# Performance work log

Hardware: AMD Instinct MI355X
Metric: run time of the kernel (lower is better)

## Reference

```python
import jax, jax.numpy as jnp
import numpy as np

NEG_SLOPE = 0.2  # PyG GATConv default negative_slope


def _add_self_loops(edge_index, num_nodes):
    # PyG GATConv add_self_loops=True default
    loop = jnp.arange(num_nodes, dtype=edge_index.dtype)
    src = jnp.concatenate([edge_index[0], loop])
    dst = jnp.concatenate([edge_index[1], loop])
    return src, dst


def _gat_layer(x, src, dst, W, att_src, att_dst, bias, heads, out_ch):
    """One PyG-style GATConv layer (concat=True).
    x: [N, F_in]; W: [F_in, heads*out_ch]; att_*: [heads, out_ch]; bias: [heads*out_ch].
    """
    N = x.shape[0]
    h = (x @ W).reshape(N, heads, out_ch)               # [N, H, C]
    a_src = jnp.einsum('nhc,hc->nh', h, att_src)        # [N, H]
    a_dst = jnp.einsum('nhc,hc->nh', h, att_dst)        # [N, H]
    logits = jax.nn.leaky_relu(a_src[src] + a_dst[dst], NEG_SLOPE)  # [E, H]
    # segment softmax over destination neighborhoods
    m = jax.ops.segment_max(logits, dst, num_segments=N)            # [N, H]
    e = jnp.exp(logits - m[dst])                                     # [E, H]
    s = jax.ops.segment_sum(e, dst, num_segments=N)                  # [N, H]
    alpha = e / s[dst]                                               # [E, H]
    # scatter-aggregate weighted source features
    out = jax.ops.segment_sum(alpha[:, :, None] * h[src], dst, num_segments=N)  # [N, H, C]
    return out.reshape(N, heads * out_ch) + bias


def setup_inputs() -> dict:
    key = jax.random.key(0)
    ks = jax.random.split(key, 10)
    N, E = 50000, 800000
    F_in, HID, H, NC = 128, 64, 4, 10
    x = jax.random.normal(ks[0], (N, F_in), dtype=jnp.float32)
    edge_index = jax.random.randint(ks[1], (2, E), 0, N, dtype=jnp.int64)
    sc1 = 1.0 / np.sqrt(F_in)
    sc2 = 1.0 / np.sqrt(HID * H)
    return {
        'x': x,
        'edge_index': edge_index,
        'W1': jax.random.normal(ks[2], (F_in, H * HID), dtype=jnp.float32) * sc1,
        'att_src1': jax.random.normal(ks[3], (H, HID), dtype=jnp.float32) * sc1,
        'att_dst1': jax.random.normal(ks[4], (H, HID), dtype=jnp.float32) * sc1,
        'b1': jnp.zeros((H * HID,), dtype=jnp.float32),
        'W2': jax.random.normal(ks[5], (H * HID, NC), dtype=jnp.float32) * sc2,
        'att_src2': jax.random.normal(ks[6], (1, NC), dtype=jnp.float32) * sc2,
        'att_dst2': jax.random.normal(ks[7], (1, NC), dtype=jnp.float32) * sc2,
        'b2': jnp.zeros((NC,), dtype=jnp.float32),
    }


def reference(x, edge_index, W1, att_src1, att_dst1, b1, W2, att_src2, att_dst2, b2):
    N = x.shape[0]
    src, dst = _add_self_loops(edge_index, N)
    h = _gat_layer(x, src, dst, W1, att_src1, att_dst1, b1, heads=4, out_ch=64)
    h = jax.nn.elu(h)
    out = _gat_layer(h, src, dst, W2, att_src2, att_dst2, b2, heads=1, out_ch=10)
    return out
```

## Files before the change

### kernel.cpp

```cpp
#include <hip/hip_runtime.h>
#include <hip/hip_fp16.h>
#include <math.h>

#define NEG_SLOPE 0.2f
#define LOG2E 1.44269504088896f

#if __has_builtin(__builtin_amdgcn_exp2f)
#define EXP2(x) __builtin_amdgcn_exp2f(x)
#else
#define EXP2(x) exp2f(x)
#endif

typedef _Float16 half8 __attribute__((ext_vector_type(8)));
typedef float floatx4 __attribute__((ext_vector_type(4)));

__global__ __launch_bounds__(256) void prep1(const float* __restrict__ W1,
                                             half8* __restrict__ Bpack,
                                             int* __restrict__ deg, int N) {
  if (blockIdx.x < 16) {
    int tid = blockIdx.x * 256 + threadIdx.x;
    int l = tid & 63;
    int ksnt = tid >> 6;
    int ks = ksnt & 3;
    int nt = ksnt >> 2;
    int col = nt * 16 + (l & 15);
    int krow = ks * 32 + (l >> 4) * 8;
    half8 v;
#pragma unroll
    for (int j = 0; j < 8; j++) v[j] = (_Float16)W1[(krow + j) * 256 + col];
    Bpack[tid] = v;
  } else {
    int i = (blockIdx.x - 16) * 256 + threadIdx.x;
    if (i < N) deg[i] = 0;
  }
}

__global__ __launch_bounds__(256) void phase2(
    const float* __restrict__ x, const half8* __restrict__ Bpack,
    const float* __restrict__ att_s, const float* __restrict__ att_d,
    __half* __restrict__ h1, float* __restrict__ a1s, float* __restrict__ a1d,
    const int* __restrict__ dst, int* __restrict__ deg, int* __restrict__ rank,
    int N, int E, int gemmBlocks, int histBlocks) {
  if ((int)blockIdx.x >= gemmBlocks) {
    int b = blockIdx.x - gemmBlocks;
    for (int e = b * 256 + threadIdx.x; e < E; e += histBlocks * 256)
      rank[e] = atomicAdd(deg + dst[e], 1);
    return;
  }
  const int wave = threadIdx.x >> 6, lane = threadIdx.x & 63;
  const int quad = lane >> 4, li = lane & 15;
  const int n0 = (blockIdx.x * 4 + wave) * 16;
  if (n0 >= N) return;
  floatx4 acc[16];
#pragma unroll
  for (int t = 0; t < 16; t++) acc[t] = (floatx4){0.f, 0.f, 0.f, 0.f};
  const float* xrow = x + (size_t)(n0 + li) * 128;
#pragma unroll
  for (int ks = 0; ks < 4; ks++) {
    float4 xa = *(const float4*)(xrow + ks * 32 + quad * 8);
    float4 xb = *(const float4*)(xrow + ks * 32 + quad * 8 + 4);
    half8 a;
    a[0] = (_Float16)xa.x; a[1] = (_Float16)xa.y;
    a[2] = (_Float16)xa.z; a[3] = (_Float16)xa.w;
    a[4] = (_Float16)xb.x; a[5] = (_Float16)xb.y;
    a[6] = (_Float16)xb.z; a[7] = (_Float16)xb.w;
#pragma unroll
    for (int nt = 0; nt < 16; nt++) {
      half8 b = Bpack[(nt * 4 + ks) * 64 + lane];
      acc[nt] = __builtin_amdgcn_mfma_f32_16x16x32_f16(a, b, acc[nt], 0, 0, 0);
    }
  }
#pragma unroll
  for (int nt = 0; nt < 16; nt++) {
#pragma unroll
    for (int r = 0; r < 4; r++) {
      h1[(size_t)(n0 + quad * 4 + r) * 256 + nt * 16 + li] = __float2half(acc[nt][r]);
    }
  }
  float as_f[16], ad_f[16];
#pragma unroll
  for (int nt = 0; nt < 16; nt++) {
    as_f[nt] = att_s[nt * 16 + li];
    ad_f[nt] = att_d[nt * 16 + li];
  }
#pragma unroll
  for (int r = 0; r < 4; r++) {
    int node = n0 + quad * 4 + r;
#pragma unroll
    for (int h = 0; h < 4; h++) {
      float vs = 0.f, vd = 0.f;
#pragma unroll
      for (int ntl = 0; ntl < 4; ntl++) {
        int nt = h * 4 + ntl;
        vs = fmaf(acc[nt][r], as_f[nt], vs);
        vd = fmaf(acc[nt][r], ad_f[nt], vd);
      }
#pragma unroll
      for (int off = 8; off > 0; off >>= 1) {
        vs += __shfl_down(vs, off, 16);
        vd += __shfl_down(vd, off, 16);
      }
      if (li == 0) {
        a1s[node * 4 + h] = vs * LOG2E;
        a1d[node * 4 + h] = vd * LOG2E;
      }
    }
  }
}

__global__ void scan_local(const int* __restrict__ deg, int* __restrict__ excl,
                           int* __restrict__ bsum, int N) {
  __shared__ int s[256];
  int i = blockIdx.x * 256 + threadIdx.x;
  int v = (i < N) ? ((deg[i] + 1 + 3) & ~3) : 0;
  s[threadIdx.x] = v;
  __syncthreads();
  for (int off = 1; off < 256; off <<= 1) {
    int t = (threadIdx.x >= off) ? s[threadIdx.x - off] : 0;
    __syncthreads();
    s[threadIdx.x] += t;
    __syncthreads();
  }
  if (i < N) excl[i] = s[threadIdx.x] - v;
  if (threadIdx.x == 255) bsum[blockIdx.x] = s[255];
}

__global__ void scan_add2(const int* __restrict__ excl, const int* __restrict__ bsum,
                          int* __restrict__ rowptr, int* __restrict__ elist,
                          int N, int nb) {
  __shared__ int s[256];
  int v = (threadIdx.x < nb) ? bsum[threadIdx.x] : 0;
  s[threadIdx.x] = v;
  __syncthreads();
  for (int off = 1; off < 256; off <<= 1) {
    int t = (threadIdx.x >= off) ? s[threadIdx.x - off] : 0;
    __syncthreads();
    s[threadIdx.x] += t;
    __syncthreads();
  }
  __syncthreads();
  int base = (blockIdx.x > 0) ? s[blockIdx.x - 1] : 0;
  int i = blockIdx.x * 256 + threadIdx.x;
  if (i < N) {
    int r = excl[i] + base;
    rowptr[i] = r;
    elist[r] = i;
  }
}

__global__ void scatter2(const int* __restrict__ src, const int* __restrict__ dst,
                         const int* __restrict__ rank, const int* __restrict__ rowptr,
                         int* __restrict__ elist, int E) {
  int e = blockIdx.x * 256 + threadIdx.x;
  if (e >= E) return;
  elist[rowptr[dst[e]] + 1 + rank[e]] = src[e];
}

__global__ __launch_bounds__(256) void agg1_fused(
    const int* __restrict__ rowptr, const int* __restrict__ degp,
    const int* __restrict__ elist, const __half* __restrict__ h1,
    const float* __restrict__ a1s, const float* __restrict__ a1d,
    const float* __restrict__ b1, const float* __restrict__ W2,
    const float* __restrict__ as2, const float* __restrict__ ad2,
    __half* __restrict__ h2, float* __restrict__ a2s, float* __restrict__ a2d,
    int N) {
  __shared__ float w2s[64 * 41];
  const int t = threadIdx.x;
  for (int i = t; i < 2560; i += 256) {
    int ch = i / 10, jj = i - ch * 10;
    w2s[(ch >> 2) * 41 + (ch & 3) * 10 + jj] = W2[i];
  }
  __syncthreads();

  const int wave = t >> 6, lane = t & 63;
  const int n = blockIdx.x * 4 + wave;
  if (n >= N) return;
  const int row = rowptr[n];
  const int deg = degp[n] + 1;
  const int* el = elist + row;
  const int hidx = lane >> 4;
  const float adh = a1d[n * 4 + hidx];

  float den = 0.f;
  float acc0 = 0.f, acc1 = 0.f, acc2 = 0.f, acc3 = 0.f;
  int j = 0;
  for (; j + 8 <= deg; j += 8) {
    int4 eA = *(const int4*)(el + j);
    int4 eB = *(const int4*)(el + j + 4);
    int ss[8] = {eA.x, eA.y, eA.z, eA.w, eB.x, eB.y, eB.z, eB.w};
    float lv[8];
    uint2 uv[8];
#pragma unroll
    for (int u = 0; u < 8; u++) {
      lv[u] = a1s[ss[u] * 4 + hidx];
      uv[u] = *(const uint2*)(h1 + (size_t)ss[u] * 256 + lane * 4);
    }
#pragma unroll
    for (int u = 0; u < 8; u++) {
      float l = lv[u] + adh;
      float e = EXP2(fmaxf(l, NEG_SLOPE * l));
      den += e;
      float2 a = __half22float2(*(const __half2*)&uv[u].x);
      float2 b = __half22float2(*(const __half2*)&uv[u].y);
      acc0 = fmaf(e, a.x, acc0); acc1 = fmaf(e, a.y, acc1);
      acc2 = fmaf(e, b.x, acc2); acc3 = fmaf(e, b.y, acc3);
    }
  }
  for (; j + 4 <= deg; j += 4) {
    int4 eA = *(const int4*)(el + j);
    int ss[4] = {eA.x, eA.y, eA.z, eA.w};
    float lv[4];
    uint2 uv[4];
#pragma unroll
    for (int u = 0; u < 4; u++) {
      lv[u] = a1s[ss[u] * 4 + hidx];
      uv[u] = *(const uint2*)(h1 + (size_t)ss[u] * 256 + lane * 4);
    }
#pragma unroll
    for (int u = 0; u < 4; u++) {
      float l = lv[u] + adh;
      float e = EXP2(fmaxf(l, NEG_SLOPE * l));
      den += e;
      float2 a = __half22float2(*(const __half2*)&uv[u].x);
      float2 b = __half22float2(*(const __half2*)&uv[u].y);
      acc0 = fmaf(e, a.x, acc0); acc1 = fmaf(e, a.y, acc1);
      acc2 = fmaf(e, b.x, acc2); acc3 = fmaf(e, b.y, acc3);
    }
  }
  for (; j < deg; j++) {
    int s0 = el[j];
    float l0 = a1s[s0 * 4 + hidx] + adh;
    uint2 u0 = *(const uint2*)(h1 + (size_t)s0 * 256 + lane * 4);
    float e0 = EXP2(fmaxf(l0, NEG_SLOPE * l0));
    den += e0;
    float2 a = __half22float2(*(const __half2*)&u0.x);
    float2 b = __half22float2(*(const __half2*)&u0.y);
    acc0 = fmaf(e0, a.x, acc0); acc1 = fmaf(e0, a.y, acc1);
    acc2 = fmaf(e0, b.x, acc2); acc3 = fmaf(e0, b.y, acc3);
  }

  float inv = 1.0f / den;
  float4 bb = *(const float4*)(b1 + lane * 4);
  float c0 = fmaf(acc0, inv, bb.x);
  float c1 = fmaf(acc1, inv, bb.y);
  float c2 = fmaf(acc2, inv, bb.z);
  float c3 = fmaf(acc3, inv, bb.w);
  c0 = c0 > 0.f ? c0 : expm1f(c0);
  c1 = c1 > 0.f ? c1 : expm1f(c1);
  c2 = c2 > 0.f ? c2 : expm1f(c2);
  c3 = c3 > 0.f ? c3 : expm1f(c3);
  const float* w0 = w2s + lane * 41;
  float p[10];
#pragma unroll
  for (int jj = 0; jj < 10; jj++)
    p[jj] = fmaf(c0, w0[jj], fmaf(c1, w0[10 + jj], fmaf(c2, w0[20 + jj], c3 * w0[30 + jj])));
#pragma unroll
  for (int jj = 0; jj < 10; jj++) {
#pragma unroll
    for (int off = 32; off > 0; off >>= 1) p[jj] += __shfl_down(p[jj], off, 64);
  }
  if (lane == 0) {
    float ds = 0.f, dd = 0.f;
#pragma unroll
    for (int jj = 0; jj < 10; jj++) {
      h2[(size_t)n * 16 + jj] = __float2half(p[jj]);
      ds = fmaf(p[jj], as2[jj], ds);
      dd = fmaf(p[jj], ad2[jj], dd);
    }
    a2s[n] = ds * LOG2E;
    a2d[n] = dd * LOG2E;
  }
}

__global__ __launch_bounds__(256) void agg2_csr(
    const int* __restrict__ rowptr, const int* __restrict__ degp,
    const int* __restrict__ elist, const __half* __restrict__ h2,
    const float* __restrict__ a2s, const float* __restrict__ a2d,
    const float* __restrict__ b2, float* __restrict__ out, int N) {
  int wave = threadIdx.x >> 6, lane = threadIdx.x & 63;
  int n = blockIdx.x * 4 + wave;
  if (n >= N) return;
  int row = rowptr[n];
  int deg = degp[n] + 1;
  const int* el = elist + row;
  float ad = a2d[n];
  int g = lane / 10;
  int c = lane - g * 10;
  float den = 0.f, acc = 0.f;
  if (g < 6) {
    int jj = g;
    for (; jj + 6 < deg; jj += 12) {
      int sA = el[jj], sB = el[jj + 6];
      float lA = a2s[sA] + ad;
      float lB = a2s[sB] + ad;
      __half hA = h2[(size_t)sA * 16 + c];
      __half hB = h2[(size_t)sB * 16 + c];
      float eA = EXP2(fmaxf(lA, NEG_SLOPE * lA));
      float eB = EXP2(fmaxf(lB, NEG_SLOPE * lB));
      den += eA + eB;
      acc = fmaf(eA, __half2float(hA), fmaf(eB, __half2float(hB), acc));
    }
    for (; jj < deg; jj += 6) {
      int s = el[jj];
      float l = a2s[s] + ad;
      float ev = EXP2(fmaxf(l, NEG_SLOPE * l));
      den += ev;
      acc = fmaf(ev, __half2float(h2[(size_t)s * 16 + c]), acc);
    }
  }
  acc += __shfl_down(acc, 30, 64);
  den += __shfl_down(den, 30, 64);
  acc += __shfl_down(acc, 10, 64) + __shfl_down(acc, 20, 64);
  den += __shfl_down(den, 10, 64) + __shfl_down(den, 20, 64);
  if (lane < 10) out[(size_t)n * 10 + lane] = acc / den + b2[lane];
}

extern "C" void kernel_launch(void* const* d_in, const int* in_sizes, int n_in,
                              void* d_out, int out_size, void* d_ws, size_t ws_size,
                              hipStream_t stream) {
  const float* x = (const float*)d_in[0];
  const int* ei = (const int*)d_in[1];
  const float* W1 = (const float*)d_in[2];
  const float* as1 = (const float*)d_in[3];
  const float* ad1 = (const float*)d_in[4];
  const float* b1 = (const float*)d_in[5];
  const float* W2 = (const float*)d_in[6];
  const float* as2 = (const float*)d_in[7];
  const float* ad2 = (const float*)d_in[8];
  const float* b2 = (const float*)d_in[9];
  float* out = (float*)d_out;

  const int N = in_sizes[0] / 128;
  const int E = in_sizes[1] / 2;
  const int* srcp = ei;
  const int* dstp = ei + E;

  char* ws = (char*)d_ws;
  size_t off = 0;
  auto alloc = [&](size_t nbytes) {
    char* p = ws + off;
    off += (nbytes + 255) & ~(size_t)255;
    return p;
  };
  __half* h1 = (__half*)alloc((size_t)N * 256 * 2);
  half8* Bpack = (half8*)alloc((size_t)4096 * 16);
  float* a1s = (float*)alloc((size_t)N * 4 * 4);
  float* a1d = (float*)alloc((size_t)N * 4 * 4);
  __half* h2 = (__half*)alloc((size_t)N * 16 * 2);
  float* a2sv = (float*)alloc((size_t)N * 4);
  float* a2dv = (float*)alloc((size_t)N * 4);
  int* deg = (int*)alloc((size_t)N * 4);
  int* excl = (int*)alloc((size_t)N * 4);
  int* bsum = (int*)alloc(256 * 4);
  int* rowptr = (int*)alloc((size_t)(N + 1) * 4);
  int* rank = (int*)alloc((size_t)E * 4);
  int* elist = (int*)alloc((size_t)(E + 4 * (size_t)N) * 4);

  const int nb = (N + 255) / 256;
  const int gemmBlocks = (N / 16 + 3) / 4;
  const int histBlocks = 512;

  prep1<<<16 + nb, 256, 0, stream>>>(W1, Bpack, deg, N);
  phase2<<<gemmBlocks + histBlocks, 256, 0, stream>>>(
      x, Bpack, as1, ad1, h1, a1s, a1d, dstp, deg, rank, N, E, gemmBlocks, histBlocks);
  scan_local<<<nb, 256, 0, stream>>>(deg, excl, bsum, N);
  scan_add2<<<nb, 256, 0, stream>>>(excl, bsum, rowptr, elist, N, nb);
  scatter2<<<(E + 255) / 256, 256, 0, stream>>>(srcp, dstp, rank, rowptr, elist, E);
  agg1_fused<<<(N + 3) / 4, 256, 0, stream>>>(rowptr, deg, elist, h1, a1s, a1d, b1,
                                              W2, as2, ad2, h2, a2sv, a2dv, N);
  agg2_csr<<<(N + 3) / 4, 256, 0, stream>>>(rowptr, deg, elist, h2, a2sv, a2dv, b2,
                                            out, N);
}
```

Measured before the change: 267.5 us.

## Quantize layer-1 features to per-node int8 and drop CSR row padding

Stores the layer-1 projected features as uint8 with a per-node scale and zero-point offset instead of fp16. This halves the bytes gathered per edge in the first aggregation, which is bandwidth-bound on random source-row reads. The offset is removed once after accumulation using the summed scaled weights. CSR rows are also no longer padded to multiples of four, so the degree comes from consecutive row pointers and the vectorized int4 index loads become scalar loads. The int8 quantization adds rounding error relative to fp16 and could exceed tolerance.

```diff
diff --git a/kernel.cpp b/kernel.cpp
--- a/kernel.cpp
+++ b/kernel.cpp
@@ -38,7 +38,8 @@
 __global__ __launch_bounds__(256) void phase2(
     const float* __restrict__ x, const half8* __restrict__ Bpack,
     const float* __restrict__ att_s, const float* __restrict__ att_d,
-    __half* __restrict__ h1, float* __restrict__ a1s, float* __restrict__ a1d,
+    unsigned char* __restrict__ h1q, float* __restrict__ hscale,
+    float* __restrict__ a1s, float* __restrict__ a1d,
     const int* __restrict__ dst, int* __restrict__ deg, int* __restrict__ rank,
     int N, int E, int gemmBlocks, int histBlocks) {
   if ((int)blockIdx.x >= gemmBlocks) {
@@ -71,10 +72,20 @@
     }
   }
 #pragma unroll
-  for (int nt = 0; nt < 16; nt++) {
-#pragma unroll
-    for (int r = 0; r < 4; r++) {
-      h1[(size_t)(n0 + quad * 4 + r) * 256 + nt * 16 + li] = __float2half(acc[nt][r]);
+  for (int r = 0; r < 4; r++) {
+    float m = 0.f;
+#pragma unroll
+    for (int nt = 0; nt < 16; nt++) m = fmaxf(m, fabsf(acc[nt][r]));
+#pragma unroll
+    for (int off = 8; off > 0; off >>= 1) m = fmaxf(m, __shfl_xor(m, off, 16));
+    m = fmaxf(m, 1e-8f);
+    float inv = 127.0f / m;
+    int node = n0 + quad * 4 + r;
+    if (li == 0) hscale[node] = m * (1.0f / 127.0f);
+#pragma unroll
+    for (int nt = 0; nt < 16; nt++) {
+      h1q[(size_t)node * 256 + nt * 16 + li] =
+          (unsigned char)(int)(fmaf(acc[nt][r], inv, 128.5f));
     }
   }
   float as_f[16], ad_f[16];
@@ -112,7 +123,7 @@
                            int* __restrict__ bsum, int N) {
   __shared__ int s[256];
   int i = blockIdx.x * 256 + threadIdx.x;
-  int v = (i < N) ? ((deg[i] + 1 + 3) & ~3) : 0;
+  int v = (i < N) ? deg[i] + 1 : 0;
   s[threadIdx.x] = v;
   __syncthreads();
   for (int off = 1; off < 256; off <<= 1) {
@@ -146,6 +157,7 @@
     rowptr[i] = r;
     elist[r] = i;
   }
+  if (blockIdx.x == 0 && threadIdx.x == 0) rowptr[N] = s[nb - 1];
 }
 
 __global__ void scatter2(const int* __restrict__ src, const int* __restrict__ dst,
@@ -157,8 +169,8 @@
 }
 
 __global__ __launch_bounds__(256) void agg1_fused(
-    const int* __restrict__ rowptr, const int* __restrict__ degp,
-    const int* __restrict__ elist, const __half* __restrict__ h1,
+    const int* __restrict__ rowptr, const int* __restrict__ elist,
+    const unsigned char* __restrict__ h1q, const float* __restrict__ hscale,
     const float* __restrict__ a1s, const float* __restrict__ a1d,
     const float* __restrict__ b1, const float* __restrict__ W2,
     const float* __restrict__ as2, const float* __restrict__ ad2,
@@ -176,68 +188,81 @@
   const int n = blockIdx.x * 4 + wave;
   if (n >= N) return;
   const int row = rowptr[n];
-  const int deg = degp[n] + 1;
+  const int deg = rowptr[n + 1] - row;
   const int* el = elist + row;
   const int hidx = lane >> 4;
   const float adh = a1d[n * 4 + hidx];
 
-  float den = 0.f;
+  float den = 0.f, T = 0.f;
   float acc0 = 0.f, acc1 = 0.f, acc2 = 0.f, acc3 = 0.f;
   int j = 0;
   for (; j + 8 <= deg; j += 8) {
-    int4 eA = *(const int4*)(el + j);
-    int4 eB = *(const int4*)(el + j + 4);
-    int ss[8] = {eA.x, eA.y, eA.z, eA.w, eB.x, eB.y, eB.z, eB.w};
-    float lv[8];
-    uint2 uv[8];
+    int ss[8];
+#pragma unroll
+    for (int u = 0; u < 8; u++) ss[u] = el[j + u];
+    float lv[8], sc[8];
+    unsigned int qv[8];
 #pragma unroll
     for (int u = 0; u < 8; u++) {
       lv[u] = a1s[ss[u] * 4 + hidx];
-      uv[u] = *(const uint2*)(h1 + (size_t)ss[u] * 256 + lane * 4);
+      sc[u] = hscale[ss[u]];
+      qv[u] = *(const unsigned int*)(h1q + (size_t)ss[u] * 256 + lane * 4);
     }
 #pragma unroll
     for (int u = 0; u < 8; u++) {
       float l = lv[u] + adh;
       float e = EXP2(fmaxf(l, NEG_SLOPE * l));
       den += e;
-      float2 a = __half22float2(*(const __half2*)&uv[u].x);
-      float2 b = __half22float2(*(const __half2*)&uv[u].y);
-      acc0 = fmaf(e, a.x, acc0); acc1 = fmaf(e, a.y, acc1);
-      acc2 = fmaf(e, b.x, acc2); acc3 = fmaf(e, b.y, acc3);
+      float se = e * sc[u];
+      T += se;
+      acc0 = fmaf((float)(qv[u] & 0xffu), se, acc0);
+      acc1 = fmaf((float)((qv[u] >> 8) & 0xffu), se, acc1);
+      acc2 = fmaf((float)((qv[u] >> 16) & 0xffu), se, acc2);
+      acc3 = fmaf((float)(qv[u] >> 24), se, acc3);
     }
   }
   for (; j + 4 <= deg; j += 4) {
-    int4 eA = *(const int4*)(el + j);
-    int ss[4] = {eA.x, eA.y, eA.z, eA.w};
-    float lv[4];
-    uint2 uv[4];
+    int ss[4];
+#pragma unroll
+    for (int u = 0; u < 4; u++) ss[u] = el[j + u];
+    float lv[4], sc[4];
+    unsigned int qv[4];
 #pragma unroll
     for (int u = 0; u < 4; u++) {
       lv[u] = a1s[ss[u] * 4 + hidx];
-      uv[u] = *(const uint2*)(h1 + (size_t)ss[u] * 256 + lane * 4);
+      sc[u] = hscale[ss[u]];
+      qv[u] = *(const unsigned int*)(h1q + (size_t)ss[u] * 256 + lane * 4);
     }
 #pragma unroll
     for (int u = 0; u < 4; u++) {
       float l = lv[u] + adh;
       float e = EXP2(fmaxf(l, NEG_SLOPE * l));
       den += e;
-      float2 a = __half22float2(*(const __half2*)&uv[u].x);
-      float2 b = __half22float2(*(const __half2*)&uv[u].y);
-      acc0 = fmaf(e, a.x, acc0); acc1 = fmaf(e, a.y, acc1);
-      acc2 = fmaf(e, b.x, acc2); acc3 = fmaf(e, b.y, acc3);
+      float se = e * sc[u];
+      T += se;
+      acc0 = fmaf((float)(qv[u] & 0xffu), se, acc0);
+      acc1 = fmaf((float)((qv[u] >> 8) & 0xffu), se, acc1);
+      acc2 = fmaf((float)((qv[u] >> 16) & 0xffu), se, acc2);
+      acc3 = fmaf((float)(qv[u] >> 24), se, acc3);
     }
   }
   for (; j < deg; j++) {
     int s0 = el[j];
     float l0 = a1s[s0 * 4 + hidx] + adh;
-    uint2 u0 = *(const uint2*)(h1 + (size_t)s0 * 256 + lane * 4);
+    float sc0 = hscale[s0];
+    unsigned int q0 = *(const unsigned int*)(h1q + (size_t)s0 * 256 + lane * 4);
     float e0 = EXP2(fmaxf(l0, NEG_SLOPE * l0));
     den += e0;
-    float2 a = __half22float2(*(const __half2*)&u0.x);
-    float2 b = __half22float2(*(const __half2*)&u0.y);
-    acc0 = fmaf(e0, a.x, acc0); acc1 = fmaf(e0, a.y, acc1);
-    acc2 = fmaf(e0, b.x, acc2); acc3 = fmaf(e0, b.y, acc3);
-  }
+    float se = e0 * sc0;
+    T += se;
+    acc0 = fmaf((float)(q0 & 0xffu), se, acc0);
+    acc1 = fmaf((float)((q0 >> 8) & 0xffu), se, acc1);
+    acc2 = fmaf((float)((q0 >> 16) & 0xffu), se, acc2);
+    acc3 = fmaf((float)(q0 >> 24), se, acc3);
+  }
+
+  float corr = 128.0f * T;
+  acc0 -= corr; acc1 -= corr; acc2 -= corr; acc3 -= corr;
 
   float inv = 1.0f / den;
   float4 bb = *(const float4*)(b1 + lane * 4);
@@ -273,15 +298,15 @@
 }
 
 __global__ __launch_bounds__(256) void agg2_csr(
-    const int* __restrict__ rowptr, const int* __restrict__ degp,
-    const int* __restrict__ elist, const __half* __restrict__ h2,
-    const float* __restrict__ a2s, const float* __restrict__ a2d,
-    const float* __restrict__ b2, float* __restrict__ out, int N) {
+    const int* __restrict__ rowptr, const int* __restrict__ elist,
+    const __half* __restrict__ h2, const float* __restrict__ a2s,
+    const float* __restrict__ a2d, const float* __restrict__ b2,
+    float* __restrict__ out, int N) {
   int wave = threadIdx.x >> 6, lane = threadIdx.x & 63;
   int n = blockIdx.x * 4 + wave;
   if (n >= N) return;
   int row = rowptr[n];
-  int deg = degp[n] + 1;
+  int deg = rowptr[n + 1] - row;
   const int* el = elist + row;
   float ad = a2d[n];
   int g = lane / 10;
@@ -342,7 +367,8 @@
     off += (nbytes + 255) & ~(size_t)255;
     return p;
   };
-  __half* h1 = (__half*)alloc((size_t)N * 256 * 2);
+  unsigned char* h1q = (unsigned char*)alloc((size_t)N * 256);
+  float* hscale = (float*)alloc((size_t)N * 4);
   half8* Bpack = (half8*)alloc((size_t)4096 * 16);
   float* a1s = (float*)alloc((size_t)N * 4 * 4);
   float* a1d = (float*)alloc((size_t)N * 4 * 4);
@@ -354,7 +380,7 @@
   int* bsum = (int*)alloc(256 * 4);
   int* rowptr = (int*)alloc((size_t)(N + 1) * 4);
   int* rank = (int*)alloc((size_t)E * 4);
-  int* elist = (int*)alloc((size_t)(E + 4 * (size_t)N) * 4);
+  int* elist = (int*)alloc((size_t)(E + (size_t)N) * 4);
 
   const int nb = (N + 255) / 256;
   const int gemmBlocks = (N / 16 + 3) / 4;
@@ -362,12 +388,12 @@
 
   prep1<<<16 + nb, 256, 0, stream>>>(W1, Bpack, deg, N);
   phase2<<<gemmBlocks + histBlocks, 256, 0, stream>>>(
-      x, Bpack, as1, ad1, h1, a1s, a1d, dstp, deg, rank, N, E, gemmBlocks, histBlocks);
+      x, Bpack, as1, ad1, h1q, hscale, a1s, a1d, dstp, deg, rank, N, E,
+      gemmBlocks, histBlocks);
   scan_local<<<nb, 256, 0, stream>>>(deg, excl, bsum, N);
   scan_add2<<<nb, 256, 0, stream>>>(excl, bsum, rowptr, elist, N, nb);
   scatter2<<<(E + 255) / 256, 256, 0, stream>>>(srcp, dstp, rank, rowptr, elist, E);
-  agg1_fused<<<(N + 3) / 4, 256, 0, stream>>>(rowptr, deg, elist, h1, a1s, a1d, b1,
-                                              W2, as2, ad2, h2, a2sv, a2dv, N);
-  agg2_csr<<<(N + 3) / 4, 256, 0, stream>>>(rowptr, deg, elist, h2, a2sv, a2dv, b2,
-                                            out, N);
-}
+  agg1_fused<<<(N + 3) / 4, 256, 0, stream>>>(rowptr, elist, h1q, hscale, a1s, a1d,
+                                              b1, W2, as2, ad2, h2, a2sv, a2dv, N);
+  agg2_csr<<<(N + 3) / 4, 256, 0, stream>>>(rowptr, elist, h2, a2sv, a2dv, b2, out, N);
+}
```

New measurement: 256.7 us. -4.1%, faster.
